# Optimization experiments

Measured on AMD Instinct MI355X. Metric: run time of the kernel, lower is better.

## Reference

```python
import jax, jax.numpy as jnp
import numpy as np
import math

D_MODEL = 1024
D_INT = 64
N_HEADS = 16
HIDDEN = 4096
DEPTH = 1
LAMBDA_INIT = 0.8 - 0.6 * math.exp(-0.3 * DEPTH)
B, S = 4, 1024


def layernorm(x, w, b, eps=1e-5):
    mu = jnp.mean(x, axis=-1, keepdims=True)
    var = jnp.mean(jnp.square(x - mu), axis=-1, keepdims=True)
    return (x - mu) * jax.lax.rsqrt(var + eps) * w + b


def setup_inputs() -> dict:
    key = jax.random.key(0)
    ks = jax.random.split(key, 16)
    s = 0.02
    inp = {
        "input_vecs": jax.random.normal(ks[0], (B, S, D_MODEL), jnp.float32),
        "mask": jnp.ones((B, S), jnp.int32),
        # per-head stacked weights (heads axis h)
        "WQ1": jax.random.normal(ks[1], (N_HEADS, D_MODEL, D_INT), jnp.float32) * s,
        "bQ1": jnp.zeros((N_HEADS, D_INT), jnp.float32),
        "WK1": jax.random.normal(ks[2], (N_HEADS, D_MODEL, D_INT), jnp.float32) * s,
        "bK1": jnp.zeros((N_HEADS, D_INT), jnp.float32),
        "WV": jax.random.normal(ks[3], (N_HEADS, D_MODEL, 2 * D_INT), jnp.float32) * s,
        "bV": jnp.zeros((N_HEADS, 2 * D_INT), jnp.float32),
        # shared per-head LayerNorm over 2*d_internal
        "lnh_w": jnp.ones((2 * D_INT,), jnp.float32),
        "lnh_b": jnp.zeros((2 * D_INT,), jnp.float32),
        "WO": jax.random.normal(ks[4], (2 * N_HEADS * D_INT, D_MODEL), jnp.float32) * s,
        "bO": jnp.zeros((D_MODEL,), jnp.float32),
        "ln1_w": jnp.ones((D_MODEL,), jnp.float32),
        "ln1_b": jnp.zeros((D_MODEL,), jnp.float32),
        "ln2_w": jnp.ones((D_MODEL,), jnp.float32),
        "ln2_b": jnp.zeros((D_MODEL,), jnp.float32),
        "W1": jax.random.normal(ks[5], (D_MODEL, HIDDEN), jnp.float32) * s,
        "b1": jnp.zeros((HIDDEN,), jnp.float32),
        "W2": jax.random.normal(ks[6], (HIDDEN, D_MODEL), jnp.float32) * s,
        "b2": jnp.zeros((D_MODEL,), jnp.float32),
        "lambda_q1": jax.random.normal(ks[7], (D_INT,), jnp.float32) * 0.1,
        "lambda_k1": jax.random.normal(ks[8], (D_INT,), jnp.float32) * 0.1,
        "lambda_q2": jax.random.normal(ks[9], (D_INT,), jnp.float32) * 0.1,
        "lambda_k2": jax.random.normal(ks[10], (D_INT,), jnp.float32) * 0.1,
    }
    return inp


def reference(input_vecs, mask, WQ1, bQ1, WK1, bK1, WV, bV, lnh_w, lnh_b,
              WO, bO, ln1_w, ln1_b, ln2_w, ln2_b, W1, b1, W2, b2,
              lambda_q1, lambda_k1, lambda_q2, lambda_k2):
    lam = (jnp.exp(jnp.dot(lambda_q1, lambda_k1))
           - jnp.exp(jnp.dot(lambda_q2, lambda_k2)) + LAMBDA_INIT)
    # NOTE: source code uses WQ1/WK1 for BOTH (Q1,K1) and (Q2,K2), so the two
    # softmax maps are identical: A = A1 - lam*A2 == (1 - lam) * A1.
    Q = jnp.einsum('bsd,hde->hbse', input_vecs, WQ1) + bQ1[:, None, None, :]
    K = jnp.einsum('bsd,hde->hbse', input_vecs, WK1) + bK1[:, None, None, :]
    V = jnp.einsum('bsd,hdv->hbsv', input_vecs, WV) + bV[:, None, None, :]
    scores = jnp.einsum('hbse,hbte->hbst', Q, K) / jnp.sqrt(jnp.float32(D_MODEL))
    scores = jnp.where(mask[None, :, None, :] == 0, -jnp.inf, scores)
    A1 = jax.nn.softmax(scores, axis=-1)       # [H,B,S,S]
    A = (1.0 - lam) * A1                        # diff of two identical maps
    O = jnp.einsum('hbst,hbtv->hbsv', A, V)     # [H,B,S,2*D_INT]
    O = layernorm(O, lnh_w, lnh_b) * (1.0 - LAMBDA_INIT)
    # concat heads along feature dim (head-major order matches torch.cat)
    O = jnp.transpose(O, (1, 2, 0, 3)).reshape(B, S, 2 * N_HEADS * D_INT)
    attn_out = O @ WO + bO
    h1 = layernorm(input_vecs + attn_out, ln1_w, ln1_b)
    ff = jax.nn.relu(h1 @ W1 + b1) @ W2 + b2
    r2 = layernorm(h1 + ff, ln2_w, ln2_b)
    return r2, A
```

## Files before the change

### kernel.cpp

```cpp
#include <hip/hip_runtime.h>
#include <stdint.h>


typedef unsigned short u16;
typedef __attribute__((ext_vector_type(4))) float   floatx4;
typedef __attribute__((ext_vector_type(8))) __bf16  bf16x8;

#define LAMBDA_INIT_F 0.35550906759096926f
#define ONE_MINUS_LI  0.6444909324090307f

#define FLAG_OUT_BF16 1
#define FLAG_RELU     2
#define FLAG_BIAS     4
#define FLAG_SCALE    8
#define FLAG_MASK     16
#define FLAG_ACCUM    32
#define FLAG_BIAS_ROW 64
#define FLAG_LNH      128

__device__ __forceinline__ float bf2f(u16 u) {
    union { unsigned int i; float f; } w; w.i = ((unsigned int)u) << 16; return w.f;
}
__device__ __forceinline__ u16 f2bf(float f) {
    union { float f; unsigned int i; } w; w.f = f;
    unsigned int x = w.i;
    unsigned int r = x + 0x7fffu + ((x >> 16) & 1u);
    return (u16)(r >> 16);
}
__device__ __forceinline__ float wred_sum(float v) {
#pragma unroll
    for (int off = 32; off > 0; off >>= 1) v += __shfl_xor(v, off, 64);
    return v;
}
__device__ __forceinline__ void gload_lds16(const u16* g, u16* l) {
    __builtin_amdgcn_global_load_lds(
        (const __attribute__((address_space(1))) unsigned int*)g,
        (__attribute__((address_space(3))) unsigned int*)l,
        16, 0, 0);
}

template <int FLAGS, int AF32, int BF32>
__global__ __launch_bounds__(256) void gemm_bt(
    const void* __restrict__ Ap, long long lda, long long sAh, long long sAb,
    const void* __restrict__ Bp, long long ldb, long long sBh, long long sBb,
    void* __restrict__ C, long long ldc, long long sCh, long long sCb,
    int K, int nb, float scale,
    const float* __restrict__ biasA, const float* __restrict__ biasB,
    int biasSplit, int biasRowStride,
    const int* __restrict__ mask, int maskS,
    const float* __restrict__ lnw, const float* __restrict__ lnb)
{
    const int z  = blockIdx.z;
    const int hz = z / nb, bz = z % nb;
    const long long aoff = hz * sAh + bz * sAb;
    const long long boff = hz * sBh + bz * sBb;
    const long long coff = hz * sCh + bz * sCb;

    __shared__ __attribute__((aligned(16))) u16 As[128 * 32];
    __shared__ __attribute__((aligned(16))) u16 Bs[128 * 32];

    const int tid  = threadIdx.x;
    const int lane = tid & 63;
    const int wid  = tid >> 6;
    const int wm   = wid >> 1, wn = wid & 1;
    const int m0   = blockIdx.y * 128;
    const int n0   = blockIdx.x * 128;
    const int sr   = tid >> 1;
    const int sc   = (tid & 1) * 16;
    const int dr   = (wid << 5) + (lane >> 2);
    const int dk   = (lane & 3) << 3;

    floatx4 acc[4][4];
#pragma unroll
    for (int i = 0; i < 4; i++)
#pragma unroll
        for (int j = 0; j < 4; j++) acc[i][j] = (floatx4){0.f, 0.f, 0.f, 0.f};

    const int lr = lane & 15;
    const int q  = lane >> 4;

    for (int k0 = 0; k0 < K; k0 += 32) {
        u16 ta[16], tb[16];
        if constexpr (AF32) {
            const float* ga = (const float*)Ap + aoff + (long long)(m0 + sr) * lda + (k0 + sc);
            float4 f0 = *(const float4*)(ga);
            float4 f1 = *(const float4*)(ga + 4);
            float4 f2 = *(const float4*)(ga + 8);
            float4 f3 = *(const float4*)(ga + 12);
            ta[0]=f2bf(f0.x); ta[1]=f2bf(f0.y); ta[2]=f2bf(f0.z); ta[3]=f2bf(f0.w);
            ta[4]=f2bf(f1.x); ta[5]=f2bf(f1.y); ta[6]=f2bf(f1.z); ta[7]=f2bf(f1.w);
            ta[8]=f2bf(f2.x); ta[9]=f2bf(f2.y); ta[10]=f2bf(f2.z); ta[11]=f2bf(f2.w);
            ta[12]=f2bf(f3.x); ta[13]=f2bf(f3.y); ta[14]=f2bf(f3.z); ta[15]=f2bf(f3.w);
        }
        if constexpr (BF32) {
            const float* gb = (const float*)Bp + boff + (long long)(n0 + sr) * ldb + (k0 + sc);
            float4 f0 = *(const float4*)(gb);
            float4 f1 = *(const float4*)(gb + 4);
            float4 f2 = *(const float4*)(gb + 8);
            float4 f3 = *(const float4*)(gb + 12);
            tb[0]=f2bf(f0.x); tb[1]=f2bf(f0.y); tb[2]=f2bf(f0.z); tb[3]=f2bf(f0.w);
            tb[4]=f2bf(f1.x); tb[5]=f2bf(f1.y); tb[6]=f2bf(f1.z); tb[7]=f2bf(f1.w);
            tb[8]=f2bf(f2.x); tb[9]=f2bf(f2.y); tb[10]=f2bf(f2.z); tb[11]=f2bf(f2.w);
            tb[12]=f2bf(f3.x); tb[13]=f2bf(f3.y); tb[14]=f2bf(f3.z); tb[15]=f2bf(f3.w);
        }
        __syncthreads();
        if constexpr (AF32) {
            *(uint4*)&As[sr * 32 + sc]     = *(uint4*)&ta[0];
            *(uint4*)&As[sr * 32 + sc + 8] = *(uint4*)&ta[8];
        } else {
            const u16* g = (const u16*)Ap + aoff + (long long)(m0 + dr) * lda + (k0 + dk);
            gload_lds16(g,              &As[wid << 10]);
            gload_lds16(g + (lda << 4), &As[(wid << 10) + 512]);
        }
        if constexpr (BF32) {
            *(uint4*)&Bs[sr * 32 + sc]     = *(uint4*)&tb[0];
            *(uint4*)&Bs[sr * 32 + sc + 8] = *(uint4*)&tb[8];
        } else {
            const u16* g = (const u16*)Bp + boff + (long long)(n0 + dr) * ldb + (k0 + dk);
            gload_lds16(g,              &Bs[wid << 10]);
            gload_lds16(g + (ldb << 4), &Bs[(wid << 10) + 512]);
        }
        __syncthreads();

        bf16x8 af[4], bfr[4];
#pragma unroll
        for (int i = 0; i < 4; i++) {
            union { uint4 u; bf16x8 v; } t;
            t.u = *(const uint4*)&As[(wm * 64 + i * 16 + lr) * 32 + q * 8];
            af[i] = t.v;
        }
#pragma unroll
        for (int j = 0; j < 4; j++) {
            union { uint4 u; bf16x8 v; } t;
            t.u = *(const uint4*)&Bs[(wn * 64 + j * 16 + lr) * 32 + q * 8];
            bfr[j] = t.v;
        }
#pragma unroll
        for (int i = 0; i < 4; i++)
#pragma unroll
            for (int j = 0; j < 4; j++)
                acc[i][j] = __builtin_amdgcn_mfma_f32_16x16x32_bf16(af[i], bfr[j], acc[i][j], 0, 0, 0);
    }

    const int rq = lane >> 4;
    const int cc = lane & 15;

    if constexpr (FLAGS & FLAG_LNH) {
        __shared__ float lnred[2][128][2];
        float s_[4][4], q_[4][4];
#pragma unroll
        for (int i = 0; i < 4; i++)
#pragma unroll
            for (int r = 0; r < 4; r++) {
                float s = 0.f, qq = 0.f;
#pragma unroll
                for (int j = 0; j < 4; j++) { float v = acc[i][j][r]; s += v; qq += v * v; }
                s_[i][r] = s; q_[i][r] = qq;
            }
#pragma unroll
        for (int off = 1; off < 16; off <<= 1)
#pragma unroll
            for (int i = 0; i < 4; i++)
#pragma unroll
                for (int r = 0; r < 4; r++) {
                    s_[i][r] += __shfl_xor(s_[i][r], off, 64);
                    q_[i][r] += __shfl_xor(q_[i][r], off, 64);
                }
        if (cc == 0) {
#pragma unroll
            for (int i = 0; i < 4; i++)
#pragma unroll
                for (int r = 0; r < 4; r++) {
                    const int row = wm * 64 + i * 16 + rq * 4 + r;
                    lnred[wn][row][0] = s_[i][r];
                    lnred[wn][row][1] = q_[i][r];
                }
        }
        __syncthreads();
#pragma unroll
        for (int i = 0; i < 4; i++)
#pragma unroll
            for (int r = 0; r < 4; r++) {
                const int row = wm * 64 + i * 16 + rq * 4 + r;
                const float sum = lnred[0][row][0] + lnred[1][row][0];
                const float sq  = lnred[0][row][1] + lnred[1][row][1];
                const float mu  = sum * (1.f / 128.f);
                const float var = sq * (1.f / 128.f) - mu * mu;
                const float inv = rsqrtf(var + 1e-5f);
#pragma unroll
                for (int j = 0; j < 4; j++) {
                    const int col = wn * 64 + j * 16 + cc;
                    const float v = ((acc[i][j][r] - mu) * inv * lnw[col] + lnb[col]) * ONE_MINUS_LI;
                    ((u16*)C)[coff + (long long)(m0 + row) * ldc + col] = f2bf(v);
                }
            }
        return;
    }

#pragma unroll
    for (int j = 0; j < 4; j++) {
        const int col = n0 + wn * 64 + j * 16 + cc;
        float cbv = 0.f;
        if constexpr (FLAGS & FLAG_BIAS)
            cbv = (col < biasSplit) ? biasA[col] : biasB[col - biasSplit];
        bool keep = true;
        if constexpr (FLAGS & FLAG_MASK) keep = (mask[bz * maskS + col] != 0);
#pragma unroll
        for (int i = 0; i < 4; i++) {
#pragma unroll
            for (int r = 0; r < 4; r++) {
                const int row = m0 + wm * 64 + i * 16 + rq * 4 + r;
                float v = acc[i][j][r];
                if constexpr (FLAGS & FLAG_SCALE) v *= scale;
                float bv = cbv;
                if constexpr (FLAGS & FLAG_BIAS_ROW) bv = biasA[hz * biasRowStride + row];
                v += bv;
                if constexpr (FLAGS & FLAG_RELU) v = fmaxf(v, 0.f);
                if constexpr (FLAGS & FLAG_MASK) { if (!keep) v = -__builtin_inff(); }
                const long long idx = coff + (long long)row * ldc + col;
                if constexpr (FLAGS & FLAG_OUT_BF16) {
                    ((u16*)C)[idx] = f2bf(v);
                } else {
                    float* Cf = (float*)C;
                    if constexpr (FLAGS & FLAG_ACCUM) v += Cf[idx];
                    Cf[idx] = v;
                }
            }
        }
    }
}

__global__ __launch_bounds__(256) void scores_softmax(
    const u16* __restrict__ QK, const int* __restrict__ mask,
    float* __restrict__ Aout,
    const float* __restrict__ lq1, const float* __restrict__ lk1,
    const float* __restrict__ lq2, const float* __restrict__ lk2)
{
    const int tid  = threadIdx.x;
    const int lane = tid & 63;
    const int w    = tid >> 6;
    const int z    = blockIdx.z;
    const int h    = z >> 2, b = z & 3;
    const int r0   = blockIdx.x << 4;

    __shared__ int   msk[1024];
    __shared__ float redM[4][16];
    __shared__ float redS[4][16];

    *(int4*)&msk[tid * 4] = *(const int4*)(mask + b * 1024 + tid * 4);

    float d1 = lq1[lane] * lk1[lane];
    float d2 = lq2[lane] * lk2[lane];
    d1 = wred_sum(d1);
    d2 = wred_sum(d2);
    const float lamscale = 1.f - (expf(d1) - expf(d2) + LAMBDA_INIT_F);

    const int sl = lane & 15;
    const int kq = lane >> 4;

    const u16* qbase = QK + (long long)(b * 1024 + r0 + sl) * 2048 + h * 64 + kq * 8;
    bf16x8 qf0, qf1;
    {
        union { uint4 u; bf16x8 v; } t;
        t.u = *(const uint4*)(qbase);      qf0 = t.v;
        t.u = *(const uint4*)(qbase + 32); qf1 = t.v;
    }
    const u16* kbase = QK + (long long)(b * 1024) * 2048 + 1024 + h * 64 + kq * 8;

    floatx4 acc[16];
    __syncthreads();

#pragma unroll
    for (int c = 0; c < 16; c++) {
        const int t = (w << 8) + (c << 4) + sl;
        union { uint4 u; bf16x8 v; } k0_, k1_;
        k0_.u = *(const uint4*)(kbase + (long long)t * 2048);
        k1_.u = *(const uint4*)(kbase + (long long)t * 2048 + 32);
        floatx4 a = (floatx4){0.f, 0.f, 0.f, 0.f};
        a = __builtin_amdgcn_mfma_f32_16x16x32_bf16(k0_.v, qf0, a, 0, 0, 0);
        a = __builtin_amdgcn_mfma_f32_16x16x32_bf16(k1_.v, qf1, a, 0, 0, 0);
        acc[c] = a;
    }

    float mx = -__builtin_inff();
#pragma unroll
    for (int c = 0; c < 16; c++) {
        const int tb_ = (w << 8) + (c << 4) + (kq << 2);
        int4 m4 = *(const int4*)&msk[tb_];
#pragma unroll
        for (int r = 0; r < 4; r++) {
            const int mv = (r == 0) ? m4.x : (r == 1) ? m4.y : (r == 2) ? m4.z : m4.w;
            float x = (mv != 0) ? acc[c][r] * 0.03125f : -__builtin_inff();
            acc[c][r] = x;
            mx = fmaxf(mx, x);
        }
    }
    mx = fmaxf(mx, __shfl_xor(mx, 16, 64));
    mx = fmaxf(mx, __shfl_xor(mx, 32, 64));
    if (lane < 16) redM[w][lane] = mx;
    __syncthreads();
    mx = fmaxf(fmaxf(redM[0][sl], redM[1][sl]), fmaxf(redM[2][sl], redM[3][sl]));

    float s = 0.f;
#pragma unroll
    for (int c = 0; c < 16; c++)
#pragma unroll
        for (int r = 0; r < 4; r++) {
            const float e = __expf(acc[c][r] - mx);
            acc[c][r] = e;
            s += e;
        }
    s += __shfl_xor(s, 16, 64);
    s += __shfl_xor(s, 32, 64);
    if (lane < 16) redS[w][lane] = s;
    __syncthreads();
    s = redS[0][sl] + redS[1][sl] + redS[2][sl] + redS[3][sl];
    const float sc = lamscale / s;

    float* obase = Aout + (long long)z * 1048576
                 + (long long)(r0 + sl) * 1024 + (w << 8) + (kq << 2);
#pragma unroll
    for (int c = 0; c < 16; c++) {
        floatx4 o = acc[c] * sc;
        *(floatx4*)(obase + (c << 4)) = o;
    }
}

__global__ void pack_x(const float* __restrict__ X, u16* __restrict__ dst)
{
    const int i = (blockIdx.x * 256 + threadIdx.x) * 4;
    float4 f = *(const float4*)(X + i);
    u16 o[4] = { f2bf(f.x), f2bf(f.y), f2bf(f.z), f2bf(f.w) };
    *(uint2*)(dst + i) = *(const uint2*)&o[0];
}

__global__ void pack_wqkt(const float* __restrict__ WQ, const float* __restrict__ WK,
                          u16* __restrict__ dst)
{
    int i = blockIdx.x * 256 + threadIdx.x;
    int k = i & 1023;
    int n = i >> 10;
    float v;
    if (n < 1024) {
        int h = n >> 6, e = n & 63;
        v = WQ[(h * 1024 + k) * 64 + e];
    } else {
        int m = n - 1024; int h = m >> 6, e = m & 63;
        v = WK[(h * 1024 + k) * 64 + e];
    }
    dst[i] = f2bf(v);
}

__global__ void pack_wvt(const float* __restrict__ WV, u16* __restrict__ dst)
{
    int i = blockIdx.x * 256 + threadIdx.x;
    int d = i & 1023;
    int v = (i >> 10) & 127;
    int h = i >> 17;
    dst[i] = f2bf(WV[(h * 1024 + d) * 128 + v]);
}

__global__ void transpose_bf(const float* __restrict__ src, u16* __restrict__ dst,
                             int rlog2, int C)
{
    long long i = (long long)blockIdx.x * 256 + threadIdx.x;
    int r = (int)(i & ((1 << rlog2) - 1));
    int c = (int)(i >> rlog2);
    dst[i] = f2bf(src[(long long)r * C + c]);
}

__global__ __launch_bounds__(256) void ln_residual(
    const float* __restrict__ xf, const u16* __restrict__ xbf,
    const float* __restrict__ addf, const u16* __restrict__ addbf,
    const float* __restrict__ w, const float* __restrict__ bb,
    u16* __restrict__ obf, float* __restrict__ of32)
{
    const int row = blockIdx.x;
    const int tid = threadIdx.x;
    const int lane = tid & 63, wid = tid >> 6;
    const long long base = (long long)row * 1024;
    float v[4];
    float s = 0.f;
#pragma unroll
    for (int i = 0; i < 4; i++) {
        const int c = tid * 4 + i;
        float x = xf ? xf[base + c] : bf2f(xbf[base + c]);
        x += addf ? addf[base + c] : bf2f(addbf[base + c]);
        v[i] = x; s += x;
    }
    __shared__ float red[8];
    s = wred_sum(s);
    if (lane == 0) red[wid] = s;
    __syncthreads();
    const float mu = (red[0] + red[1] + red[2] + red[3]) * (1.f / 1024.f);
    float ss = 0.f;
#pragma unroll
    for (int i = 0; i < 4; i++) { const float d = v[i] - mu; ss += d * d; }
    ss = wred_sum(ss);
    if (lane == 0) red[wid + 4] = ss;
    __syncthreads();
    const float var = (red[4] + red[5] + red[6] + red[7]) * (1.f / 1024.f);
    const float inv = rsqrtf(var + 1e-5f);
#pragma unroll
    for (int i = 0; i < 4; i++) {
        const int c = tid * 4 + i;
        const float o = (v[i] - mu) * inv * w[c] + bb[c];
        if (obf) obf[base + c] = f2bf(o);
        else     of32[base + c] = o;
    }
}

extern "C" void kernel_launch(void* const* d_in, const int* in_sizes, int n_in,
                              void* d_out, int out_size, void* d_ws, size_t ws_size,
                              hipStream_t stream)
{
    const float* X     = (const float*)d_in[0];
    const int*   mask  = (const int*)d_in[1];
    const float* WQ1   = (const float*)d_in[2];
    const float* bQ1   = (const float*)d_in[3];
    const float* WK1   = (const float*)d_in[4];
    const float* bK1   = (const float*)d_in[5];
    const float* WV    = (const float*)d_in[6];
    const float* bV    = (const float*)d_in[7];
    const float* lnh_w = (const float*)d_in[8];
    const float* lnh_b = (const float*)d_in[9];
    const float* WO    = (const float*)d_in[10];
    const float* bO    = (const float*)d_in[11];
    const float* ln1_w = (const float*)d_in[12];
    const float* ln1_b = (const float*)d_in[13];
    const float* ln2_w = (const float*)d_in[14];
    const float* ln2_b = (const float*)d_in[15];
    const float* W1    = (const float*)d_in[16];
    const float* b1    = (const float*)d_in[17];
    const float* W2    = (const float*)d_in[18];
    const float* b2    = (const float*)d_in[19];
    const float* lq1   = (const float*)d_in[20];
    const float* lk1   = (const float*)d_in[21];
    const float* lq2   = (const float*)d_in[22];
    const float* lk2   = (const float*)d_in[23];

    float* r2   = (float*)d_out;
    float* Aout = (float*)d_out + 4194304;
    u16*   Vt   = (u16*)d_out;
    float* ff2  = (float*)d_out;

    uint8_t* wp = (uint8_t*)d_ws;
    const size_t MB = 1024 * 1024;
    u16*   WqkT = (u16*)(wp + 0);
    u16*   WvT  = (u16*)(wp + 4 * MB);
    u16*   QK   = (u16*)(wp + 8 * MB);
    u16*   Xbf  = (u16*)(wp + 24 * MB);
    u16*   WOt  = (u16*)(wp + 0);
    u16*   Ocat = (u16*)(wp + 24 * MB);
    u16*   attnb= (u16*)(wp + 8 * MB);
    u16*   h1   = (u16*)(wp + 40 * MB);
    u16*   W1t  = (u16*)(wp + 16 * MB);
    u16*   W2t  = (u16*)(wp + 32 * MB);
    u16*   ff1c = (u16*)(wp + 0);
    (void)ws_size; (void)in_sizes; (void)n_in; (void)out_size;

    const long long Z = 0;
    const int NOSPLIT = 1 << 30;

    pack_x<<<4096, 256, 0, stream>>>(X, Xbf);
    pack_wqkt<<<8192, 256, 0, stream>>>(WQ1, WK1, WqkT);
    pack_wvt<<<8192, 256, 0, stream>>>(WV, WvT);

    gemm_bt<FLAG_OUT_BF16 | FLAG_BIAS, 0, 0><<<dim3(16, 32, 1), 256, 0, stream>>>(
        Xbf, 1024, Z, Z, WqkT, 1024, Z, Z, QK, 2048, Z, Z,
        1024, 1, 1.f, bQ1, bK1, 1024, 0, nullptr, 0, nullptr, nullptr);

    gemm_bt<FLAG_OUT_BF16 | FLAG_BIAS_ROW, 0, 0><<<dim3(8, 1, 64), 256, 0, stream>>>(
        WvT, 1024, 131072LL, Z, Xbf, 1024, Z, 1048576LL,
        Vt, 1024, 524288LL, 131072LL,
        1024, 4, 1.f, bV, nullptr, NOSPLIT, 128, nullptr, 0, nullptr, nullptr);

    transpose_bf<<<8192, 256, 0, stream>>>(WO, WOt, 11, 1024);

    scores_softmax<<<dim3(64, 1, 64), 256, 0, stream>>>(QK, mask, Aout,
                                                        lq1, lk1, lq2, lk2);

    gemm_bt<FLAG_LNH, 1, 0><<<dim3(1, 8, 64), 256, 0, stream>>>(
        Aout, 1024, 4194304LL, 1048576LL, Vt, 1024, 524288LL, 131072LL,
        Ocat, 2048, 128LL, 2097152LL,
        1024, 4, 1.f, nullptr, nullptr, NOSPLIT, 0, nullptr, 0, lnh_w, lnh_b);

    gemm_bt<FLAG_OUT_BF16 | FLAG_BIAS, 0, 0><<<dim3(8, 32, 1), 256, 0, stream>>>(
        Ocat, 2048, Z, Z, WOt, 2048, Z, Z, attnb, 1024, Z, Z,
        2048, 1, 1.f, bO, nullptr, NOSPLIT, 0, nullptr, 0, nullptr, nullptr);

    ln_residual<<<4096, 256, 0, stream>>>(X, nullptr, nullptr, attnb,
                                          ln1_w, ln1_b, h1, nullptr);

    transpose_bf<<<16384, 256, 0, stream>>>(W1, W1t, 10, 4096);
    transpose_bf<<<16384, 256, 0, stream>>>(W2, W2t, 12, 1024);

    for (int c = 0; c < 2; c++) {
        gemm_bt<FLAG_OUT_BF16 | FLAG_BIAS | FLAG_RELU, 0, 0><<<dim3(16, 32, 1), 256, 0, stream>>>(
            h1, 1024, Z, Z, W1t + (long long)c * 2097152, 1024, Z, Z,
            ff1c, 2048, Z, Z,
            1024, 1, 1.f, b1 + c * 2048, nullptr, NOSPLIT, 0, nullptr, 0, nullptr, nullptr);
        if (c == 0) {
            gemm_bt<FLAG_BIAS, 0, 0><<<dim3(8, 32, 1), 256, 0, stream>>>(
                ff1c, 2048, Z, Z, W2t + c * 2048, 4096, Z, Z, ff2, 1024, Z, Z,
                2048, 1, 1.f, b2, nullptr, NOSPLIT, 0, nullptr, 0, nullptr, nullptr);
        } else {
            gemm_bt<FLAG_ACCUM, 0, 0><<<dim3(8, 32, 1), 256, 0, stream>>>(
                ff1c, 2048, Z, Z, W2t + c * 2048, 4096, Z, Z, ff2, 1024, Z, Z,
                2048, 1, 1.f, nullptr, nullptr, NOSPLIT, 0, nullptr, 0, nullptr, nullptr);
        }
    }

    ln_residual<<<4096, 256, 0, stream>>>(nullptr, h1, ff2, nullptr,
                                          ln2_w, ln2_b, nullptr, r2);
}
```

Measured before the change: 901.5 us.

## Double GEMM K-tile to 64 and XOR-swizzle LDS layout to avoid bank conflicts

The GEMM main loop now stages a 64-wide K slice per iteration instead of 32, which halves the number of barrier pairs and loop iterations per output tile. The LDS tiles are stored with an XOR swizzle on 8-element column chunks, keyed by row, so the MFMA fragment reads and the direct global-to-LDS loads avoid bank conflicts. In exchange, shared memory use doubles to 32 KB per block and more registers hold the fp32-to-bf16 staging buffers, which may lower occupancy. It also assumes K is a multiple of 64.

```diff
diff --git a/kernel.cpp b/kernel.cpp
--- a/kernel.cpp
+++ b/kernel.cpp
@@ -37,6 +37,14 @@
         (const __attribute__((address_space(1))) unsigned int*)g,
         (__attribute__((address_space(3))) unsigned int*)l,
         16, 0, 0);
+}
+__device__ __forceinline__ void ld32f_bf(const float* g, u16* o) {
+#pragma unroll
+    for (int m = 0; m < 8; m++) {
+        float4 f = *(const float4*)(g + m * 4);
+        o[m * 4 + 0] = f2bf(f.x); o[m * 4 + 1] = f2bf(f.y);
+        o[m * 4 + 2] = f2bf(f.z); o[m * 4 + 3] = f2bf(f.w);
+    }
 }
 
 template <int FLAGS, int AF32, int BF32>
@@ -56,8 +64,8 @@
     const long long boff = hz * sBh + bz * sBb;
     const long long coff = hz * sCh + bz * sCb;
 
-    __shared__ __attribute__((aligned(16))) u16 As[128 * 32];
-    __shared__ __attribute__((aligned(16))) u16 Bs[128 * 32];
+    __shared__ __attribute__((aligned(16))) u16 As[128 * 64];
+    __shared__ __attribute__((aligned(16))) u16 Bs[128 * 64];
 
     const int tid  = threadIdx.x;
     const int lane = tid & 63;
@@ -66,9 +74,10 @@
     const int m0   = blockIdx.y * 128;
     const int n0   = blockIdx.x * 128;
     const int sr   = tid >> 1;
-    const int sc   = (tid & 1) * 16;
-    const int dr   = (wid << 5) + (lane >> 2);
-    const int dk   = (lane & 3) << 3;
+    const int sh   = (tid & 1) * 32;
+    const int srx  = (sr & 7) << 3;
+    const int drow = lane >> 3;
+    const int dcol = ((lane & 7) ^ drow) << 3;
 
     floatx4 acc[4][4];
 #pragma unroll
@@ -76,70 +85,63 @@
 #pragma unroll
         for (int j = 0; j < 4; j++) acc[i][j] = (floatx4){0.f, 0.f, 0.f, 0.f};
 
-    const int lr = lane & 15;
-    const int q  = lane >> 4;
-
-    for (int k0 = 0; k0 < K; k0 += 32) {
-        u16 ta[16], tb[16];
-        if constexpr (AF32) {
-            const float* ga = (const float*)Ap + aoff + (long long)(m0 + sr) * lda + (k0 + sc);
-            float4 f0 = *(const float4*)(ga);
-            float4 f1 = *(const float4*)(ga + 4);
-            float4 f2 = *(const float4*)(ga + 8);
-            float4 f3 = *(const float4*)(ga + 12);
-            ta[0]=f2bf(f0.x); ta[1]=f2bf(f0.y); ta[2]=f2bf(f0.z); ta[3]=f2bf(f0.w);
-            ta[4]=f2bf(f1.x); ta[5]=f2bf(f1.y); ta[6]=f2bf(f1.z); ta[7]=f2bf(f1.w);
-            ta[8]=f2bf(f2.x); ta[9]=f2bf(f2.y); ta[10]=f2bf(f2.z); ta[11]=f2bf(f2.w);
-            ta[12]=f2bf(f3.x); ta[13]=f2bf(f3.y); ta[14]=f2bf(f3.z); ta[15]=f2bf(f3.w);
-        }
-        if constexpr (BF32) {
-            const float* gb = (const float*)Bp + boff + (long long)(n0 + sr) * ldb + (k0 + sc);
-            float4 f0 = *(const float4*)(gb);
-            float4 f1 = *(const float4*)(gb + 4);
-            float4 f2 = *(const float4*)(gb + 8);
-            float4 f3 = *(const float4*)(gb + 12);
-            tb[0]=f2bf(f0.x); tb[1]=f2bf(f0.y); tb[2]=f2bf(f0.z); tb[3]=f2bf(f0.w);
-            tb[4]=f2bf(f1.x); tb[5]=f2bf(f1.y); tb[6]=f2bf(f1.z); tb[7]=f2bf(f1.w);
-            tb[8]=f2bf(f2.x); tb[9]=f2bf(f2.y); tb[10]=f2bf(f2.z); tb[11]=f2bf(f2.w);
-            tb[12]=f2bf(f3.x); tb[13]=f2bf(f3.y); tb[14]=f2bf(f3.z); tb[15]=f2bf(f3.w);
-        }
+    const int lr   = lane & 15;
+    const int q    = lane >> 4;
+    const int rxor = (lr & 7) << 3;
+
+    for (int k0 = 0; k0 < K; k0 += 64) {
+        union { u16 u[32]; uint4 v[4]; } ta, tb;
+        if constexpr (AF32)
+            ld32f_bf((const float*)Ap + aoff + (long long)(m0 + sr) * lda + k0 + sh, ta.u);
+        if constexpr (BF32)
+            ld32f_bf((const float*)Bp + boff + (long long)(n0 + sr) * ldb + k0 + sh, tb.u);
         __syncthreads();
         if constexpr (AF32) {
-            *(uint4*)&As[sr * 32 + sc]     = *(uint4*)&ta[0];
-            *(uint4*)&As[sr * 32 + sc + 8] = *(uint4*)&ta[8];
+#pragma unroll
+            for (int m = 0; m < 4; m++)
+                *(uint4*)&As[sr * 64 + ((sh + m * 8) ^ srx)] = ta.v[m];
         } else {
-            const u16* g = (const u16*)Ap + aoff + (long long)(m0 + dr) * lda + (k0 + dk);
-            gload_lds16(g,              &As[wid << 10]);
-            gload_lds16(g + (lda << 4), &As[(wid << 10) + 512]);
+            const u16* g = (const u16*)Ap + aoff
+                         + (long long)(m0 + (wid << 5) + drow) * lda + k0 + dcol;
+#pragma unroll
+            for (int j = 0; j < 4; j++)
+                gload_lds16(g + (long long)(j * 8) * lda, &As[((wid << 5) + j * 8) * 64]);
         }
         if constexpr (BF32) {
-            *(uint4*)&Bs[sr * 32 + sc]     = *(uint4*)&tb[0];
-            *(uint4*)&Bs[sr * 32 + sc + 8] = *(uint4*)&tb[8];
+#pragma unroll
+            for (int m = 0; m < 4; m++)
+                *(uint4*)&Bs[sr * 64 + ((sh + m * 8) ^ srx)] = tb.v[m];
         } else {
-            const u16* g = (const u16*)Bp + boff + (long long)(n0 + dr) * ldb + (k0 + dk);
-            gload_lds16(g,              &Bs[wid << 10]);
-            gload_lds16(g + (ldb << 4), &Bs[(wid << 10) + 512]);
+            const u16* g = (const u16*)Bp + boff
+                         + (long long)(n0 + (wid << 5) + drow) * ldb + k0 + dcol;
+#pragma unroll
+            for (int j = 0; j < 4; j++)
+                gload_lds16(g + (long long)(j * 8) * ldb, &Bs[((wid << 5) + j * 8) * 64]);
         }
         __syncthreads();
 
-        bf16x8 af[4], bfr[4];
-#pragma unroll
-        for (int i = 0; i < 4; i++) {
-            union { uint4 u; bf16x8 v; } t;
-            t.u = *(const uint4*)&As[(wm * 64 + i * 16 + lr) * 32 + q * 8];
-            af[i] = t.v;
-        }
-#pragma unroll
-        for (int j = 0; j < 4; j++) {
-            union { uint4 u; bf16x8 v; } t;
-            t.u = *(const uint4*)&Bs[(wn * 64 + j * 16 + lr) * 32 + q * 8];
-            bfr[j] = t.v;
-        }
-#pragma unroll
-        for (int i = 0; i < 4; i++)
-#pragma unroll
-            for (int j = 0; j < 4; j++)
-                acc[i][j] = __builtin_amdgcn_mfma_f32_16x16x32_bf16(af[i], bfr[j], acc[i][j], 0, 0, 0);
+#pragma unroll
+        for (int ks = 0; ks < 2; ks++) {
+            const int cb = ks * 32 + q * 8;
+            bf16x8 af[4], bfr[4];
+#pragma unroll
+            for (int i = 0; i < 4; i++) {
+                union { uint4 u; bf16x8 v; } t;
+                t.u = *(const uint4*)&As[(wm * 64 + i * 16 + lr) * 64 + (cb ^ rxor)];
+                af[i] = t.v;
+            }
+#pragma unroll
+            for (int j = 0; j < 4; j++) {
+                union { uint4 u; bf16x8 v; } t;
+                t.u = *(const uint4*)&Bs[(wn * 64 + j * 16 + lr) * 64 + (cb ^ rxor)];
+                bfr[j] = t.v;
+            }
+#pragma unroll
+            for (int i = 0; i < 4; i++)
+#pragma unroll
+                for (int j = 0; j < 4; j++)
+                    acc[i][j] = __builtin_amdgcn_mfma_f32_16x16x32_bf16(af[i], bfr[j], acc[i][j], 0, 0, 0);
+        }
     }
 
     const int rq = lane >> 4;
```

Result: no change. 884.3 us (-1.9%).
